# Kernel tuning notes

Measured on AMD Instinct MI355X. Metric: run time of the kernel, lower is better.

The kernel has to match this reference:

```python
import jax, jax.numpy as jnp
from jax import lax
import numpy as np

B, A, T = 128, 32, 32
HID = 64
DEG = 7
MODES = 25
OUT_FRAMES = 12
NHEAD, DHEAD = 16, 64


def legendre_tmat(out_frames, degree):
    # normalized Legendre basis evaluated at t_n, shape [degree+1, len(t_n)]
    t = np.arange(-6, out_frames + 1, dtype=np.float32)
    t = t / t[-1]
    P = [np.ones_like(t), t]
    for n in range(1, degree):
        P.append(((2 * n + 1) * t * P[n] - n * P[n - 1]) / (n + 1))
    P = np.stack(P[: degree + 1], 0)
    norm = np.sqrt((2 * np.arange(degree + 1) + 1) / 2.0).astype(np.float32)
    return (P * norm[:, None]).astype(np.float32)


def _conv(x, w, stride, pad):
    return lax.conv_general_dilated(x, w, (stride, stride), [(pad, pad), (pad, pad)],
                                    dimension_numbers=("NCHW", "OIHW", "NCHW"))


def _bn(x, g, b, eps=1e-5):
    m = jnp.mean(x, axis=(0, 2, 3), keepdims=True)
    v = jnp.var(x, axis=(0, 2, 3), keepdims=True)
    return (x - m) / jnp.sqrt(v + eps) * g[None, :, None, None] + b[None, :, None, None]


def setup_inputs() -> dict:
    key = jax.random.key(0)
    ks = jax.random.split(key, 32)

    def rn(i, shape, scale=0.05):
        return jax.random.normal(ks[i], shape, dtype=jnp.float32) * scale

    inp = {
        "cnn_feat": rn(0, (B, 1024, 14, 14), 1.0),
        "ego_state": rn(1, (B, T, 5), 1.0),
        "agents_state": rn(2, (B, A, T, 5), 1.0),
        "ego_state_len": jax.random.randint(ks[3], (B,), 0, T),
        "agents_state_len": jax.random.randint(ks[4], (B, A), 0, T),
        "agents_grid_pos": jax.random.randint(ks[5], (B, A, 2), 0, 14),
        "state_fc_W": rn(6, (HID, 5)), "state_fc_b": rn(7, (HID,)),
        "lstm_Wih": rn(8, (4 * HID, HID)), "lstm_Whh": rn(9, (4 * HID, HID)),
        "lstm_bih": rn(10, (4 * HID,)), "lstm_bhh": rn(11, (4 * HID,)),
        "enc_fc_W": rn(12, (HID, HID)), "enc_fc_b": rn(13, (HID,)),
        "conv1_W": rn(14, (512, 1024 + HID, 3, 3)),
        "bn1_g": jnp.ones((512,), jnp.float32), "bn1_b": jnp.zeros((512,), jnp.float32),
        "conv2_W": rn(15, (512, 512, 3, 3)),
        "bn2_g": jnp.ones((512,), jnp.float32), "bn2_b": jnp.zeros((512,), jnp.float32),
        "q_W": rn(16, (NHEAD * DHEAD, 512 + HID)),
        "k_W": rn(17, (NHEAD * DHEAD, 512, 1, 1)),
        "v_W": rn(18, (NHEAD * DHEAD, 512, 1, 1)),
        "attn_out_W": rn(19, (512, NHEAD * DHEAD)), "attn_out_b": rn(20, (512,)),
        "cls_W": rn(21, (MODES, 512 + HID + 512)), "cls_b": rn(22, (MODES,)),
        "dec1_W": rn(23, (256, 512 + HID + 512)), "dec1_b": rn(24, (256,)),
        "dec2_W": rn(25, ((DEG + 1) * 2 * MODES, 256)), "dec2_b": rn(26, ((DEG + 1) * 2 * MODES,)),
    }
    return inp


def reference(cnn_feat, ego_state, agents_state, ego_state_len, agents_state_len,
              agents_grid_pos, state_fc_W, state_fc_b, lstm_Wih, lstm_Whh, lstm_bih,
              lstm_bhh, enc_fc_W, enc_fc_b, conv1_W, bn1_g, bn1_b, conv2_W, bn2_g,
              bn2_b, q_W, k_W, v_W, attn_out_W, attn_out_b, cls_W, cls_b, dec1_W,
              dec1_b, dec2_W, dec2_b):
    Bn, _, Hs, Ws = cnn_feat.shape

    def lstm_encode(seq, lens):
        # seq [N,T,5]; packed-sequence semantics with zero init == take h at step len-1
        N, Tn, _ = seq.shape
        h = seq @ state_fc_W.T + state_fc_b  # [N,T,64]

        def step(carry, xt):
            hh, cc = carry
            g = xt @ lstm_Wih.T + hh @ lstm_Whh.T + lstm_bih + lstm_bhh
            i, f_, gg, o = jnp.split(g, 4, axis=-1)
            cc = jax.nn.sigmoid(f_) * cc + jax.nn.sigmoid(i) * jnp.tanh(gg)
            hh = jax.nn.sigmoid(o) * jnp.tanh(cc)
            return (hh, cc), hh

        z = jnp.zeros((N, HID), h.dtype)
        _, hs = lax.scan(step, (z, z), h.transpose(1, 0, 2))  # hs [T,N,64]
        idx = jnp.clip(lens, 1, Tn).astype(jnp.int32) - 1
        last = hs[idx, jnp.arange(N)]
        return last @ enc_fc_W.T + enc_fc_b

    ego = lstm_encode(ego_state, ego_state_len)  # [B,64]
    ag = lstm_encode(agents_state.reshape(Bn * A, T, 5),
                     agents_state_len.reshape(-1)).reshape(Bn, A, HID)

    # scatter-add agent encodings into the spatial grid (overlapping writes accumulate)
    grid = jnp.zeros((Bn, Hs, Ws, HID), cnn_feat.dtype)
    bidx = jnp.broadcast_to(jnp.arange(Bn)[:, None], (Bn, A))
    grid = grid.at[bidx, agents_grid_pos[..., 0], agents_grid_pos[..., 1]].add(ag)

    x = jnp.concatenate([cnn_feat, grid.transpose(0, 3, 1, 2)], axis=1)
    x = jax.nn.relu(_bn(_conv(x, conv1_W, 1, 1), bn1_g, bn1_b))
    x = jax.nn.relu(_bn(_conv(x, conv2_W, 2, 1), bn2_g, bn2_b))  # [B,512,7,7]

    ego_t = jnp.concatenate([x[:, :, 3, 3], ego], axis=1)  # [B,576]
    q = (ego_t @ q_W.T).reshape(Bn, NHEAD, DHEAD)
    k = _conv(x, k_W, 1, 1).reshape(Bn, NHEAD, DHEAD, -1)  # g = 9*9 = 81
    v = _conv(x, v_W, 1, 1).reshape(Bn, NHEAD, DHEAD, -1)
    energy = jnp.einsum("bhf,bhfg->bhg", q, k)
    attn = jax.nn.softmax(energy / (NHEAD * DHEAD) ** 0.5, axis=2)
    o = jnp.einsum("bhg,bhdg->bhd", attn, v).reshape(Bn, -1)
    o = o @ attn_out_W.T + attn_out_b

    feat = jnp.concatenate([o, ego_t], axis=1)  # [B,1088]
    conf = feat @ cls_W.T + cls_b
    d = jax.nn.relu(feat @ dec1_W.T + dec1_b)
    d = (d @ dec2_W.T + dec2_b).reshape(Bn, MODES, -1)

    tmat = jnp.asarray(legendre_tmat(OUT_FRAMES, DEG))  # [DEG+1, 19]
    out_x = d[:, :, : DEG + 1] @ tmat
    out_y = d[:, :, DEG + 1:] @ tmat
    traj = jnp.stack([out_x, out_y], axis=3)  # [B,MODES,19,2]
    return traj, conf
```

## Files before the change

kernel.cpp:

```cpp
#include <hip/hip_runtime.h>
#include <stdint.h>
#include <stddef.h>

#define DEVINL static __device__ __forceinline__

typedef __attribute__((ext_vector_type(8))) short  bfrag;
typedef __attribute__((ext_vector_type(4))) float  facc;

DEVINL uint16_t f2b(float f){
  uint32_t u = __float_as_uint(f);
  return (uint16_t)((u + 0x7fffu + ((u >> 16) & 1u)) >> 16);
}
DEVINL float b2f(uint16_t b){ return __uint_as_float(((uint32_t)b) << 16); }

DEVINL facc MFMA(bfrag a, bfrag b, facc c){
  return __builtin_amdgcn_mfma_f32_16x16x32_bf16(a, b, c, 0, 0, 0);
}

DEVINL void gload16(const void* g, void* l){
  __builtin_amdgcn_global_load_lds(
      (const __attribute__((address_space(1))) uint32_t*)g,
      (__attribute__((address_space(3))) uint32_t*)l, 16, 0, 0);
}

DEVINL float fast_tanh(float x){
  return 2.f/(1.f+__expf(-2.f*x)) - 1.f;
}

struct F2BJobs {
  const float* s[7];
  uint16_t*    d[7];
  int          n[7];
};
__global__ void k_f2b_multi(F2BJobs jobs){
  int j = blockIdx.y;
  const float* s = jobs.s[j];
  uint16_t* d = jobs.d[j];
  int n = jobs.n[j];
  int i = blockIdx.x*256 + threadIdx.x;
  int st = gridDim.x*256;
  for(; i<n; i+=st) d[i] = f2b(s[i]);
}

__global__ void k_zborder(uint16_t* __restrict__ X, uint16_t* __restrict__ Y){
  int b = blockIdx.x & 127, t = threadIdx.x;
  uint16_t* base = (blockIdx.x < 128) ? X : Y;
  int C = (blockIdx.x < 128) ? 1088 : 512;
  for(int p=0;p<60;p++){
    int y, x;
    if(p<16){ y=0; x=p; }
    else if(p<32){ y=15; x=p-16; }
    else { int q=p-32; y=1+(q>>1); x=(q&1)?15:0; }
    uint32_t* dst = (uint32_t*)(base + ((size_t)(b*16+y)*16 + x)*C);
    for(int i=t;i<C/2;i+=256) dst[i] = 0;
  }
}

__global__ void k_lstm_prep(const float* __restrict__ Wih, const float* __restrict__ Whh,
                            const float* __restrict__ bih, const float* __restrict__ bhh,
                            const float* __restrict__ sW, const float* __restrict__ sb,
                            const float* __restrict__ encW,
                            uint16_t* __restrict__ Wc, float* __restrict__ be,
                            uint16_t* __restrict__ encWb, float* __restrict__ tm){
  int n = threadIdx.x;
  if(n < 19){
    float tv = (float)(n - 6) / 12.0f;
    float Pm = 1.0f, Pc = tv;
    tm[0*19+n] = Pm * sqrtf(0.5f);
    tm[1*19+n] = Pc * sqrtf(1.5f);
    for(int q=1; q<7; q++){
      float Pn = ((float)(2*q+1)*tv*Pc - (float)q*Pm) / (float)(q+1);
      Pm = Pc; Pc = Pn;
      tm[(q+1)*19+n] = Pc * sqrtf((float)(2*(q+1)+1) * 0.5f);
    }
  }
  for(int k=0;k<64;k++) Wc[n*96+k] = f2b(Whh[n*64+k]);
  for(int k5=0;k5<5;k5++){
    float s = 0.f;
    for(int j=0;j<64;j++) s += Wih[n*64+j]*sW[j*5+k5];
    Wc[n*96+64+k5] = f2b(s);
  }
  for(int k=69;k<96;k++) Wc[n*96+k] = 0;
  float s = 0.f;
  for(int j=0;j<64;j++) s += Wih[n*64+j]*sb[j];
  be[n] = s + bih[n] + bhh[n];
  if(n < 64){
    for(int k=0;k<64;k++) encWb[n*64+k] = f2b(encW[n*64+k]);
  }
}

__global__ __launch_bounds__(256) void k_lstm(
    const float* __restrict__ ego_seq, const float* __restrict__ ag_seq,
    const int* __restrict__ ego_len, const int* __restrict__ ag_len,
    const int* __restrict__ grid_pos,
    const uint16_t* __restrict__ Wc, const float* __restrict__ be,
    const uint16_t* __restrict__ encWb, const float* __restrict__ encB,
    float* __restrict__ agrid, uint16_t* __restrict__ egoT, uint16_t* __restrict__ feat)
{
  __shared__ __align__(16) uint16_t A[32*96];
  __shared__ float Xf[32*160];
  __shared__ int   idxs[32];

  int t = threadIdx.x, w = t>>6, l = t&63;
  int blk = blockIdx.x;
  bool isEgo = blk < 4;
  int seq0 = isEgo ? blk*32 : (blk-4)*32;
  const float* seqp = (isEgo ? ego_seq : ag_seq) + (size_t)seq0*160;

  for(int i=t;i<32*160;i+=256) Xf[i] = seqp[i];
  if(t < 32){
    int L = isEgo ? ego_len[seq0+t] : ag_len[seq0+t];
    if(L < 1) L = 1;
    idxs[t] = L-1;
  }
  for(int i=t;i<32*96;i+=256) A[i] = 0;

  bfrag bf[4][3];
  float be4[4];
  for(int ct=0;ct<4;ct++){
    int n = (ct*4+w)*16 + (l&15);
    for(int ks=0;ks<3;ks++)
      bf[ct][ks] = *(const bfrag*)(Wc + n*96 + ks*32 + (l>>4)*8);
    be4[ct] = be[n];
  }
  float cst[8], hl[8];
  for(int i=0;i<8;i++){ cst[i]=0.f; hl[i]=0.f; }
  __syncthreads();
  int myidx[8];
  for(int rt=0;rt<2;rt++) for(int r=0;r<4;r++){
    int s = rt*16 + (l>>4)*4 + r;
    myidx[rt*4+r] = idxs[s];
  }

  for(int st=0; st<32; st++){
    if(t < 160){ int s=t/5, kk=t%5; A[s*96+64+kk] = f2b(Xf[s*160 + st*5 + kk]); }
    __syncthreads();
    facc acc[2][4];
    for(int rt=0;rt<2;rt++) for(int ct=0;ct<4;ct++) acc[rt][ct] = facc{0.f,0.f,0.f,0.f};
    #pragma unroll
    for(int ks=0;ks<3;ks++){
      bfrag aA[2];
      #pragma unroll
      for(int rt=0;rt<2;rt++)
        aA[rt] = *(const bfrag*)(A + (rt*16+(l&15))*96 + ks*32 + (l>>4)*8);
      #pragma unroll
      for(int rt=0;rt<2;rt++)
        #pragma unroll
        for(int ct=0;ct<4;ct++)
          acc[rt][ct] = MFMA(aA[rt], bf[ct][ks], acc[rt][ct]);
    }
    __syncthreads();
    #pragma unroll
    for(int rt=0;rt<2;rt++) for(int r=0;r<4;r++){
      int cell = rt*4+r;
      int s = rt*16 + (l>>4)*4 + r;
      float gi = acc[rt][0][r] + be4[0];
      float gf = acc[rt][1][r] + be4[1];
      float gg = acc[rt][2][r] + be4[2];
      float go = acc[rt][3][r] + be4[3];
      float si = 1.f/(1.f+__expf(-gi));
      float sf = 1.f/(1.f+__expf(-gf));
      float so = 1.f/(1.f+__expf(-go));
      float tg = fast_tanh(gg);
      float c2 = sf*cst[cell] + si*tg;
      cst[cell] = c2;
      float hn = so*fast_tanh(c2);
      A[s*96 + w*16 + (l&15)] = f2b(hn);
      if(st == myidx[cell]) hl[cell] = hn;
    }
  }
  __syncthreads();
  for(int rt=0;rt<2;rt++) for(int r=0;r<4;r++){
    int s = rt*16 + (l>>4)*4 + r;
    A[s*96 + w*16 + (l&15)] = f2b(hl[rt*4+r]);
  }
  __syncthreads();
  bfrag eb[2];
  for(int ks=0;ks<2;ks++)
    eb[ks] = *(const bfrag*)(encWb + (w*16+(l&15))*64 + ks*32 + (l>>4)*8);
  facc ea[2]; ea[0] = facc{0.f,0.f,0.f,0.f}; ea[1] = facc{0.f,0.f,0.f,0.f};
  for(int ks=0;ks<2;ks++){
    for(int rt=0;rt<2;rt++){
      bfrag aA = *(const bfrag*)(A + (rt*16+(l&15))*96 + ks*32 + (l>>4)*8);
      ea[rt] = MFMA(aA, eb[ks], ea[rt]);
    }
  }
  int n = w*16 + (l&15);
  float bn_ = encB[n];
  for(int rt=0;rt<2;rt++) for(int r=0;r<4;r++){
    int s = rt*16 + (l>>4)*4 + r;
    float v = ea[rt][r] + bn_;
    int gs = seq0 + s;
    if(isEgo){
      egoT[(size_t)gs*576 + 512 + n] = f2b(v);
      feat[(size_t)gs*1088 + 1024 + n] = f2b(v);
    } else {
      int py = grid_pos[gs*2+0], px = grid_pos[gs*2+1];
      atomicAdd(&agrid[((size_t)(gs>>5)*196 + py*14 + px)*64 + n], v);
    }
  }
}

__global__ void k_packx(const float* __restrict__ cnn, const float* __restrict__ agrid,
                        uint16_t* __restrict__ Xp)
{
  __shared__ float tile[32*200];
  int b = blockIdx.x, ch = blockIdx.y, t = threadIdx.x;
  if(ch < 32){
    int c0 = ch*32;
    for(int i=t;i<32*196;i+=256){
      int ci = i/196, s = i%196;
      tile[ci*200+s] = cnn[((size_t)b*1024 + c0+ci)*196 + s];
    }
    __syncthreads();
    for(int i=t;i<32*196;i+=256){
      int s = i>>5, ci = i&31;
      int y = s/14, x = s%14;
      Xp[(((size_t)b*16 + y+1)*16 + x+1)*1088 + c0 + ci] = f2b(tile[ci*200+s]);
    }
  } else {
    int j0 = (ch-32)*32;
    for(int i=t;i<32*196;i+=256){
      int s = i>>5, ji = i&31;
      int y = s/14, x = s%14;
      Xp[(((size_t)b*16 + y+1)*16 + x+1)*1088 + 1024 + j0 + ji] =
          f2b(agrid[((size_t)b*196 + s)*64 + j0 + ji]);
    }
  }
}

__global__ void k_packw(const float* __restrict__ W, uint16_t* __restrict__ Wp, int O, int C)
{
  int o = blockIdx.x;
  int c = blockIdx.y*64 + threadIdx.x;
  const float* src = W + ((size_t)o*C + c)*9;
  float v[9];
  #pragma unroll
  for(int d=0;d<9;d++) v[d] = src[d];
  #pragma unroll
  for(int d=0;d<9;d++)
    Wp[((size_t)d*O + o)*C + c] = f2b(v[d]);
}

__global__ void k_packw2(const float* __restrict__ W, uint16_t* __restrict__ Wp)
{
  int o = blockIdx.x;
  int c = blockIdx.y*64 + threadIdx.x;
  const float* src = W + ((size_t)o*512 + c)*9;
  float v[9];
  #pragma unroll
  for(int d=0;d<9;d++) v[d] = src[d];
  #pragma unroll
  for(int dy=0;dy<3;dy++)
    #pragma unroll
    for(int dx=0;dx<3;dx++)
      Wp[((size_t)(dy*512 + o))*1536 + dx*512 + c] = f2b(v[dy*3+dx]);
}

__global__ __launch_bounds__(512) void k_conv1_8p(
    const uint16_t* __restrict__ Ain, const uint16_t* __restrict__ Wb,
    uint16_t* __restrict__ Out, float* __restrict__ stats)
{
  constexpr int CB = 1088;
  constexpr int NSTEP = 153;
  __shared__ __align__(16) char LDSb[131072];

  int t = threadIdx.x, w = t>>6, l = t&63;
  int wm = w>>2, wn = w&3;

  int xcd = blockIdx.x & 7, pos = blockIdx.x >> 3;
  int wgid = (xcd < 4 ? xcd*25 : 100 + (xcd-4)*24) + pos;
  int m0 = (wgid % 98) * 256;
  int n0 = (wgid / 98) * 256;

  const uint16_t* aP[2][2];
  const uint16_t* bP[2][2];
  #pragma unroll
  for(int P=0;P<2;P++)
    #pragma unroll
    for(int j=0;j<2;j++){
      int partrow = j*64 + (t>>3);
      int swz = ((t&7) ^ (partrow&7))*8;
      int gr = P*64 + partrow + ((partrow>=64)?64:0);
      int m = m0 + gr; int b = m/196, s = m%196, y = s/14, x = s%14;
      aP[P][j] = Ain + ((b*16+y)*16+x)*CB + swz;
      int nb = n0 + (partrow>>5)*64 + P*32 + (partrow&31);
      bP[P][j] = Wb + (size_t)nb*CB + swz;
    }

  facc acc[8][4];
  #pragma unroll
  for(int i=0;i<8;i++)
    #pragma unroll
    for(int j=0;j<4;j++) acc[i][j] = facc{0.f,0.f,0.f,0.f};

  int dd = 0;

  #define STG(buf, PART) do{                                                   \
    if((PART)==0 || (PART)==3){ const int P_ = ((PART)==3);                    \
      _Pragma("unroll")                                                        \
      for(int j_=0;j_<2;j_++)                                                  \
        gload16(aP[P_][j_], LDSb + (buf)*65536 + P_*16384 + j_*8192 + w*1024); \
    } else { const int P_ = ((PART)==2);                                       \
      _Pragma("unroll")                                                        \
      for(int j_=0;j_<2;j_++)                                                  \
        gload16(bP[P_][j_], LDSb + (buf)*65536 + 32768 + P_*16384 + j_*8192 + w*1024); \
    }                                                                          \
  }while(0)

  #define ADVK() do{                                                          \
    if(dd==8){                                                                \
      _Pragma("unroll")                                                       \
      for(int P_=0;P_<2;P_++) for(int j_=0;j_<2;j_++){                        \
        aP[P_][j_] += 64 - 34*CB; bP[P_][j_] += 64 - 8*512*CB; }              \
      dd = 0;                                                                 \
    } else {                                                                  \
      int sA_ = (dd==2||dd==5) ? 14*CB : CB;                                  \
      _Pragma("unroll")                                                       \
      for(int P_=0;P_<2;P_++) for(int j_=0;j_<2;j_++){                        \
        aP[P_][j_] += sA_; bP[P_][j_] += 512*CB; }                            \
      dd++;                                                                   \
    }                                                                         \
  }while(0)

  #define VM4 asm volatile("s_waitcnt vmcnt(4)" ::: "memory")
  #define VM2 asm volatile("s_waitcnt vmcnt(2)" ::: "memory")
  #define VM0 asm volatile("s_waitcnt vmcnt(0)" ::: "memory")

  #define PHASE(mh, nh, SP, DO_STG, WAIT) do{                                 \
    const uint16_t* Ab_ = (const uint16_t*)(LDSb + p*65536 + (mh)*16384);     \
    const uint16_t* Bb_ = (const uint16_t*)(LDSb + p*65536 + 32768 + (nh)*16384); \
    bfrag a_[4][2], b_[2][2];                                                 \
    _Pragma("unroll")                                                         \
    for(int i_=0;i_<4;i_++)                                                   \
      _Pragma("unroll")                                                       \
      for(int ks_=0;ks_<2;ks_++)                                              \
        a_[i_][ks_] = *(const bfrag*)(Ab_ + (wm*64 + i_*16 + (l&15))*64       \
                        + ((ks_*32 + (l>>4)*8) ^ ((l&7)<<3)));                \
    _Pragma("unroll")                                                         \
    for(int j_=0;j_<2;j_++)                                                   \
      _Pragma("unroll")                                                       \
      for(int ks_=0;ks_<2;ks_++)                                              \
        b_[j_][ks_] = *(const bfrag*)(Bb_ + (wn*32 + j_*16 + (l&15))*64       \
                        + ((ks_*32 + (l>>4)*8) ^ ((l&7)<<3)));                \
    if(DO_STG) STG(p^1, SP);                                                  \
    __builtin_amdgcn_sched_barrier(0);                                        \
    __builtin_amdgcn_s_barrier();                                             \
    __builtin_amdgcn_s_setprio(1);                                            \
    _Pragma("unroll")                                                         \
    for(int ks_=0;ks_<2;ks_++)                                                \
      _Pragma("unroll")                                                       \
      for(int i_=0;i_<4;i_++)                                                 \
        _Pragma("unroll")                                                     \
        for(int j_=0;j_<2;j_++)                                               \
          acc[(mh)*4+i_][(nh)*2+j_] =                                         \
            MFMA(a_[i_][ks_], b_[j_][ks_], acc[(mh)*4+i_][(nh)*2+j_]);        \
    __builtin_amdgcn_s_setprio(0);                                            \
    WAIT;                                                                     \
    __builtin_amdgcn_s_barrier();                                             \
  }while(0)

  STG(0,0); STG(0,1); STG(0,2); STG(0,3);
  ADVK();
  VM4;
  __builtin_amdgcn_s_barrier();

  for(int kt=0; kt<NSTEP-1; kt++){
    int p = kt&1;
    PHASE(0,0, 0, 1, VM4);
    PHASE(0,1, 1, 1, VM4);
    PHASE(1,0, 2, 1, (void)0);
    PHASE(1,1, 3, 1, VM4);
    if(kt < NSTEP-2) ADVK();
  }
  {
    int p = 0;
    PHASE(0,0, 0, 0, VM2);
    PHASE(0,1, 1, 0, VM0);
    PHASE(1,0, 2, 0, (void)0);
    PHASE(1,1, 3, 0, (void)0);
  }

  #undef PHASE
  #undef STG
  #undef ADVK

  __syncthreads();
  int* oo = (int*)LDSb;
  if(t < 256){
    int m = m0 + t; int b = m/196, s = m%196, y = s/14, x = s%14;
    oo[t] = ((b*16 + y+1)*16 + (x+1))*512;
  }
  __syncthreads();
  #pragma unroll
  for(int i=0;i<8;i++)
    #pragma unroll
    for(int j=0;j<4;j++){
      int n = n0 + wn*64 + j*16 + (l&15);
      #pragma unroll
      for(int r=0;r<4;r++){
        int mr = wm*128 + i*16 + (l>>4)*4 + r;
        Out[(size_t)oo[mr] + n] = f2b(acc[i][j][r]);
      }
    }
  __syncthreads();
  float* sred = (float*)LDSb;
  int rg = wm*4 + (l>>4);
  #pragma unroll
  for(int j=0;j<4;j++){
    float s=0.f, q=0.f;
    #pragma unroll
    for(int i=0;i<8;i++)
      #pragma unroll
      for(int r=0;r<4;r++){ float v = acc[i][j][r]; s += v; q += v*v; }
    int nl = wn*64 + j*16 + (l&15);
    sred[(nl*8 + rg)*2+0] = s;
    sred[(nl*8 + rg)*2+1] = q;
  }
  __syncthreads();
  if(t < 256){
    float s=0.f, q=0.f;
    #pragma unroll
    for(int rgi=0;rgi<8;rgi++){ s += sred[(t*8+rgi)*2]; q += sred[(t*8+rgi)*2+1]; }
    atomicAdd(&stats[n0+t], s);
    atomicAdd(&stats[512+n0+t], q);
  }
}

__global__ __launch_bounds__(256) void k_conv2dy(
    const uint16_t* __restrict__ Ain, const uint16_t* __restrict__ Wb,
    float* __restrict__ PS)
{
  __shared__ __align__(16) uint16_t As[128*64];
  __shared__ __align__(16) uint16_t Bs[128*64];

  int t = threadIdx.x, w = t>>6, l = t&63;
  int dy = blockIdx.y;

  int xcd = blockIdx.x & 7, pos = blockIdx.x >> 3;
  int wgid = (xcd < 4 ? xcd*25 : 100 + (xcd-4)*24) + pos;
  int n0 = (wgid / 49) * 128;
  int m0 = (wgid % 49) * 128;

  const uint16_t* aP[4];
  const uint16_t* bP[4];
  #pragma unroll
  for(int p=0;p<4;p++){
    int r = w*32 + p*8 + (l>>3);
    int m = m0 + r;
    int b = m/49, s = m%49, y = s/7, x = s%7;
    aP[p] = Ain + ((b*16 + 2*y + dy)*16 + 2*x)*512 + (l&7)*8;
    bP[p] = Wb + ((size_t)(dy*512 + n0 + r))*1536 + (l&7)*8;
  }

  facc acc[4][4];
  #pragma unroll
  for(int i=0;i<4;i++)
    #pragma unroll
    for(int j=0;j<4;j++) acc[i][j] = facc{0.f,0.f,0.f,0.f};
  int wm = w>>1, wn = w&1;
  char* asDst = (char*)As + w*4096;
  char* bsDst = (char*)Bs + w*4096;

  for(int stp=0; stp<24; stp++){
    #pragma unroll
    for(int p=0;p<4;p++){ gload16(aP[p], asDst + p*1024); aP[p] += 64; }
    #pragma unroll
    for(int p=0;p<4;p++){ gload16(bP[p], bsDst + p*1024); bP[p] += 64; }
    __syncthreads();
    #pragma unroll
    for(int ks=0;ks<2;ks++){
      bfrag a[4], b[4];
      #pragma unroll
      for(int i=0;i<4;i++)
        a[i] = *(const bfrag*)(As + (wm*64 + i*16 + (l&15))*64 + ks*32 + (l>>4)*8);
      #pragma unroll
      for(int j=0;j<4;j++)
        b[j] = *(const bfrag*)(Bs + (wn*64 + j*16 + (l&15))*64 + ks*32 + (l>>4)*8);
      #pragma unroll
      for(int i=0;i<4;i++)
        #pragma unroll
        for(int j=0;j<4;j++)
          acc[i][j] = MFMA(a[i], b[j], acc[i][j]);
    }
    __syncthreads();
  }

  float* out = PS + (size_t)dy*3211264;
  #pragma unroll
  for(int i=0;i<4;i++)
    #pragma unroll
    for(int j=0;j<4;j++){
      int n = n0 + wn*64 + j*16 + (l&15);
      #pragma unroll
      for(int r=0;r<4;r++){
        int mr = m0 + wm*64 + i*16 + (l>>4)*4 + r;
        out[(size_t)mr*512 + n] = acc[i][j][r];
      }
    }
}

__global__ void k_bn2sum(const float* __restrict__ PS, uint16_t* __restrict__ Y2,
                         float* __restrict__ stats)
{
  int t = threadIdx.x;
  int m0 = blockIdx.x*128;
  float s0=0,s1=0,q0=0,q1=0;
  for(int i=0;i<128;i++){
    size_t off = (size_t)(m0+i)*512 + 2*t;
    float2 p0 = *(const float2*)(PS + off);
    float2 p1 = *(const float2*)(PS + 3211264 + off);
    float2 p2 = *(const float2*)(PS + 6422528 + off);
    float a = p0.x+p1.x+p2.x, c = p0.y+p1.y+p2.y;
    s0+=a; q0+=a*a; s1+=c; q1+=c*c;
    *(uint32_t*)(Y2 + off) = (uint32_t)f2b(a) | ((uint32_t)f2b(c)<<16);
  }
  atomicAdd(&stats[2*t],   s0);
  atomicAdd(&stats[2*t+1], s1);
  atomicAdd(&stats[512+2*t],   q0);
  atomicAdd(&stats[512+2*t+1], q1);
}

__global__ __launch_bounds__(256) void k_convkv(
    const uint16_t* __restrict__ Ain, const uint16_t* __restrict__ Wb,
    uint16_t* __restrict__ Out)
{
  constexpr int CB = 512;
  constexpr int NB = 2048;
  constexpr int NWG = 49*16;
  constexpr int Q8 = NWG/8;

  __shared__ __align__(16) uint16_t As[128*64];
  __shared__ __align__(16) uint16_t Bs[128*64];

  int t = threadIdx.x, w = t>>6, l = t&63;

  int xcd = blockIdx.x & 7, pos = blockIdx.x >> 3;
  int wgid = xcd*Q8 + pos;
  int n0 = (wgid / 49) * 128;
  int m0 = (wgid % 49) * 128;

  const uint16_t* aP[4];
  const uint16_t* bP[4];
  #pragma unroll
  for(int p=0;p<4;p++){
    int r = w*32 + p*8 + (l>>3);
    aP[p] = Ain + (size_t)(m0 + r)*512 + (l&7)*8;
    bP[p] = Wb + (size_t)(n0 + r)*CB + (l&7)*8;
  }

  facc acc[4][4];
  #pragma unroll
  for(int i=0;i<4;i++)
    #pragma unroll
    for(int j=0;j<4;j++) acc[i][j] = facc{0.f,0.f,0.f,0.f};
  int wm = w>>1, wn = w&1;
  char* asDst = (char*)As + w*4096;
  char* bsDst = (char*)Bs + w*4096;

  for(int cc=0; cc<8; cc++){
    #pragma unroll
    for(int p=0;p<4;p++){ gload16(aP[p], asDst + p*1024); aP[p] += 64; }
    #pragma unroll
    for(int p=0;p<4;p++){ gload16(bP[p], bsDst + p*1024); bP[p] += 64; }
    __syncthreads();
    #pragma unroll
    for(int ks=0;ks<2;ks++){
      bfrag a[4], b[4];
      #pragma unroll
      for(int i=0;i<4;i++)
        a[i] = *(const bfrag*)(As + (wm*64 + i*16 + (l&15))*64 + ks*32 + (l>>4)*8);
      #pragma unroll
      for(int j=0;j<4;j++)
        b[j] = *(const bfrag*)(Bs + (wn*64 + j*16 + (l&15))*64 + ks*32 + (l>>4)*8);
      #pragma unroll
      for(int i=0;i<4;i++)
        #pragma unroll
        for(int j=0;j<4;j++)
          acc[i][j] = MFMA(a[i], b[j], acc[i][j]);
    }
    __syncthreads();
  }

  #pragma unroll
  for(int i=0;i<4;i++)
    #pragma unroll
    for(int j=0;j<4;j++){
      int n = n0 + wn*64 + j*16 + (l&15);
      #pragma unroll
      for(int r=0;r<4;r++){
        int mr = m0 + wm*64 + i*16 + (l>>4)*4 + r;
        Out[(size_t)mr*2048 + n] = f2b(acc[i][j][r]);
      }
    }
}

template<int PAD>
__global__ void k_bnapply(uint16_t* __restrict__ Y, const float* __restrict__ stats,
                          const float* __restrict__ gg, const float* __restrict__ bb,
                          int M, float invM,
                          uint16_t* __restrict__ egoT, uint16_t* __restrict__ feat)
{
  int t = threadIdx.x;
  int m0 = blockIdx.x*8;
  float mu0 = stats[2*t]*invM,       mu1 = stats[2*t+1]*invM;
  float v0 = stats[512+2*t]*invM - mu0*mu0, v1 = stats[512+2*t+1]*invM - mu1*mu1;
  float sc0 = gg[2*t]  *rsqrtf(v0+1e-5f), sc1 = gg[2*t+1]*rsqrtf(v1+1e-5f);
  float sh0 = bb[2*t]   - mu0*sc0,        sh1 = bb[2*t+1] - mu1*sc1;
  for(int i=0;i<8;i++){
    int m = m0+i; if(m>=M) break;
    size_t off;
    if(PAD){ int b=m/196, s=m%196, y=s/14, x=s%14; off = (((size_t)b*16+y+1)*16 + x+1)*512; }
    else off = (size_t)m*512;
    uint32_t u = *(const uint32_t*)(Y + off + 2*t);
    float a = fmaxf(b2f((uint16_t)u)*sc0 + sh0, 0.f);
    float c = fmaxf(b2f((uint16_t)(u>>16))*sc1 + sh1, 0.f);
    uint32_t pu = (uint32_t)f2b(a) | ((uint32_t)f2b(c)<<16);
    *(uint32_t*)(Y + off + 2*t) = pu;
    if(!PAD && (m%49)==24){
      int b = m/49;
      *(uint32_t*)(egoT + (size_t)b*576 + 2*t) = pu;
      *(uint32_t*)(feat + (size_t)b*1088 + 512 + 2*t) = pu;
    }
  }
}

__global__ __launch_bounds__(256) void k_sgemm(
    const uint16_t* __restrict__ A, int lda,
    const uint16_t* __restrict__ B, int ldb,
    const float* __restrict__ bias,
    void* __restrict__ C, int ldc,
    int N, int K, int flags)
{
  int t = threadIdx.x, w = t>>6, l = t&63;
  int nt = blockIdx.x*4 + w;
  int n  = nt*16 + (l&15);
  int m0 = blockIdx.y*16;
  bool nv = n < N;
  facc acc = facc{0.f,0.f,0.f,0.f};
  for(int k=0;k<K;k+=32){
    bfrag af = *(const bfrag*)(A + (size_t)(m0+(l&15))*lda + k + (l>>4)*8);
    bfrag bf_ = {0,0,0,0,0,0,0,0};
    if(nv) bf_ = *(const bfrag*)(B + (size_t)n*ldb + k + (l>>4)*8);
    acc = MFMA(af, bf_, acc);
  }
  if(nv){
    float bv = bias ? bias[n] : 0.f;
    #pragma unroll
    for(int r=0;r<4;r++){
      int m = m0 + (l>>4)*4 + r;
      float v = acc[r] + bv;
      if(flags & 1) v = fmaxf(v, 0.f);
      if(flags & 2) ((float*)C)[(size_t)m*ldc + n] = v;
      else ((uint16_t*)C)[(size_t)m*ldc + n] = f2b(v);
    }
  }
}

__global__ __launch_bounds__(256) void k_attn(
    const float* __restrict__ q, const uint16_t* __restrict__ kv,
    uint16_t* __restrict__ o)
{
  int t = threadIdx.x, w = t>>6, l = t&63;
  int idx = blockIdx.x*4 + w;
  int b = idx>>4, h = idx&15;
  float qf = q[(size_t)b*1024 + h*64 + l];
  const uint16_t* kp = kv + (size_t)b*49*2048 + h*64 + l;
  float eo = 0.f;
  for(int g=0; g<49; g++){
    float p = qf * b2f(kp[(size_t)g*2048]);
    for(int s=32;s>0;s>>=1) p += __shfl_xor(p, s);
    if(l == g) eo = p;
  }
  float e = (l<49) ? eo*(1.f/32.f) : -1e30f;
  float mx = e;
  for(int s=32;s>0;s>>=1) mx = fmaxf(mx, __shfl_xor(mx, s));
  mx = fmaxf(mx, 0.f);
  float p = (l<49) ? __expf(e-mx) : 0.f;
  float den = p;
  for(int s=32;s>0;s>>=1) den += __shfl_xor(den, s);
  den += 32.f*__expf(-mx);
  const uint16_t* vp = kv + (size_t)b*49*2048 + 1024 + h*64 + l;
  float accv = 0.f;
  for(int g=0; g<49; g++){
    float pg = __shfl(p, g);
    accv += pg * b2f(vp[(size_t)g*2048]);
  }
  o[(size_t)b*1024 + h*64 + l] = f2b(accv/den);
}

__global__ void k_traj(const float* __restrict__ d2, const float* __restrict__ tm,
                       float* __restrict__ out)
{
  int i = blockIdx.x*256 + threadIdx.x;
  if(i >= 3200) return;
  const float* dp = d2 + (size_t)i*16;
  float cx[8], cy[8];
  #pragma unroll
  for(int j=0;j<8;j++){ cx[j]=dp[j]; cy[j]=dp[8+j]; }
  float* op = out + (size_t)i*38;
  for(int tt=0;tt<19;tt++){
    float x=0.f, y=0.f;
    #pragma unroll
    for(int j=0;j<8;j++){ float tv = tm[j*19+tt]; x += cx[j]*tv; y += cy[j]*tv; }
    op[tt*2+0]=x; op[tt*2+1]=y;
  }
}

extern "C" void kernel_launch(void* const* d_in, const int* in_sizes, int n_in,
                              void* d_out, int out_size, void* d_ws, size_t ws_size,
                              hipStream_t stream)
{
  const float* cnn      = (const float*)d_in[0];
  const float* ego_seq  = (const float*)d_in[1];
  const float* ag_seq   = (const float*)d_in[2];
  const int*   ego_len  = (const int*)d_in[3];
  const int*   ag_len   = (const int*)d_in[4];
  const int*   grid_pos = (const int*)d_in[5];
  const float* sW  = (const float*)d_in[6];
  const float* sb  = (const float*)d_in[7];
  const float* Wih = (const float*)d_in[8];
  const float* Whh = (const float*)d_in[9];
  const float* bih = (const float*)d_in[10];
  const float* bhh = (const float*)d_in[11];
  const float* encW = (const float*)d_in[12];
  const float* encB = (const float*)d_in[13];
  const float* conv1W = (const float*)d_in[14];
  const float* bn1g = (const float*)d_in[15];
  const float* bn1b = (const float*)d_in[16];
  const float* conv2W = (const float*)d_in[17];
  const float* bn2g = (const float*)d_in[18];
  const float* bn2b = (const float*)d_in[19];
  const float* qWf  = (const float*)d_in[20];
  const float* kWf  = (const float*)d_in[21];
  const float* vWf  = (const float*)d_in[22];
  const float* aoW  = (const float*)d_in[23];
  const float* aoB  = (const float*)d_in[24];
  const float* clsWf = (const float*)d_in[25];
  const float* clsB  = (const float*)d_in[26];
  const float* d1Wf  = (const float*)d_in[27];
  const float* d1B   = (const float*)d_in[28];
  const float* d2Wf  = (const float*)d_in[29];
  const float* d2B   = (const float*)d_in[30];

  char* ws = (char*)d_ws;
  const size_t XP_OFF   = 0;
  const size_t PS_OFF   = 0;
  const size_t KV_OFF   = 0;
  const size_t Y2_OFF   = 41943040;
  const size_t Y1P_OFF  = 71303168;
  const size_t WP1_OFF  = 104857600;
  const size_t WP2_OFF  = 114884608;
  const size_t WKV_OFF  = 119603200;
  const size_t QW_OFF   = 121700352;
  const size_t AOW_OFF  = 122880000;
  const size_t CLSW_OFF = 123928576;
  const size_t D1W_OFF  = 123982976;
  const size_t D2W_OFF  = 124540032;
  const size_t GRID_OFF = 124744832;
  const size_t EGOT_OFF = 131167360;
  const size_t FEAT_OFF = 131314816;
  const size_t QBUF_OFF = 131593344;
  const size_t OBUF_OFF = 132117632;
  const size_t D1_OFF   = 132379776;
  const size_t D2_OFF   = 132445312;
  const size_t WC_OFF   = 132650112;
  const size_t BE_OFF   = 132699264;
  const size_t ENCW_OFF = 132700288;
  const size_t TMAT_OFF = 132708480;
  const size_t ST1_OFF  = 132709120;
  const size_t ST2_OFF  = 132713216;

  uint16_t* XP   = (uint16_t*)(ws + XP_OFF);
  float*    PS   = (float*)(ws + PS_OFF);
  uint16_t* KV   = (uint16_t*)(ws + KV_OFF);
  uint16_t* Y2   = (uint16_t*)(ws + Y2_OFF);
  uint16_t* Y1P  = (uint16_t*)(ws + Y1P_OFF);
  uint16_t* WP1  = (uint16_t*)(ws + WP1_OFF);
  uint16_t* WP2  = (uint16_t*)(ws + WP2_OFF);
  uint16_t* WKV  = (uint16_t*)(ws + WKV_OFF);
  uint16_t* QW   = (uint16_t*)(ws + QW_OFF);
  uint16_t* AOW  = (uint16_t*)(ws + AOW_OFF);
  uint16_t* CLSW = (uint16_t*)(ws + CLSW_OFF);
  uint16_t* D1W  = (uint16_t*)(ws + D1W_OFF);
  uint16_t* D2W  = (uint16_t*)(ws + D2W_OFF);
  float*    GRIDB= (float*)(ws + GRID_OFF);
  uint16_t* EGOT = (uint16_t*)(ws + EGOT_OFF);
  uint16_t* FEAT = (uint16_t*)(ws + FEAT_OFF);
  float*    QBUF = (float*)(ws + QBUF_OFF);
  uint16_t* OBUF = (uint16_t*)(ws + OBUF_OFF);
  uint16_t* D1B  = (uint16_t*)(ws + D1_OFF);
  float*    D2B  = (float*)(ws + D2_OFF);
  uint16_t* WC   = (uint16_t*)(ws + WC_OFF);
  float*    BE   = (float*)(ws + BE_OFF);
  uint16_t* ENCWB= (uint16_t*)(ws + ENCW_OFF);
  float*    TMAT = (float*)(ws + TMAT_OFF);
  float*    ST1  = (float*)(ws + ST1_OFF);
  float*    ST2  = (float*)(ws + ST2_OFF);
  float*    outF = (float*)d_out;

  (void)hipMemsetAsync(ws + GRID_OFF, 0, 6422528, stream);
  (void)hipMemsetAsync(ws + ST1_OFF,  0, 8192, stream);

  k_zborder<<<256,256,0,stream>>>(XP, Y1P);

  k_lstm_prep<<<1,256,0,stream>>>(Wih,Whh,bih,bhh,sW,sb,encW, WC,BE,ENCWB, TMAT);
  k_packw<<<dim3(512,17),64,0,stream>>>(conv1W, WP1, 512, 1088);
  k_packw2<<<dim3(512,8),64,0,stream>>>(conv2W, WP2);
  {
    F2BJobs jb;
    jb.s[0]=kWf;  jb.d[0]=WKV;              jb.n[0]=1024*512;
    jb.s[1]=vWf;  jb.d[1]=WKV + 1024*512;   jb.n[1]=1024*512;
    jb.s[2]=qWf;  jb.d[2]=QW;               jb.n[2]=1024*576;
    jb.s[3]=aoW;  jb.d[3]=AOW;              jb.n[3]=512*1024;
    jb.s[4]=clsWf;jb.d[4]=CLSW;             jb.n[4]=25*1088;
    jb.s[5]=d1Wf; jb.d[5]=D1W;              jb.n[5]=256*1088;
    jb.s[6]=d2Wf; jb.d[6]=D2W;              jb.n[6]=400*256;
    k_f2b_multi<<<dim3(48,7),256,0,stream>>>(jb);
  }

  k_lstm<<<132,256,0,stream>>>(ego_seq, ag_seq, ego_len, ag_len, grid_pos,
                               WC, BE, ENCWB, encB, GRIDB, EGOT, FEAT);
  k_packx<<<dim3(128,34),256,0,stream>>>(cnn, GRIDB, XP);
  k_conv1_8p<<<196,512,0,stream>>>(XP, WP1, Y1P, ST1);
  k_bnapply<1><<<3136,256,0,stream>>>(Y1P, ST1, bn1g, bn1b, 25088, 1.f/25088.f, nullptr, nullptr);
  k_conv2dy<<<dim3(196,3),256,0,stream>>>(Y1P, WP2, PS);
  k_bn2sum<<<49,256,0,stream>>>(PS, Y2, ST2);
  k_bnapply<0><<<784,256,0,stream>>>(Y2, ST2, bn2g, bn2b, 6272, 1.f/6272.f, EGOT, FEAT);
  k_convkv<<<784,256,0,stream>>>(Y2, WKV, KV);
  k_sgemm<<<dim3(16,8),256,0,stream>>>(EGOT, 576, QW, 576, nullptr, QBUF, 1024, 1024, 576, 2);
  k_attn<<<512,256,0,stream>>>(QBUF, KV, OBUF);
  k_sgemm<<<dim3(8,8),256,0,stream>>>(OBUF, 1024, AOW, 1024, aoB, FEAT, 1088, 512, 1024, 0);
  k_sgemm<<<dim3(1,8),256,0,stream>>>(FEAT, 1088, CLSW, 1088, clsB, outF + 121600, 25, 25, 1088, 2);
  k_sgemm<<<dim3(4,8),256,0,stream>>>(FEAT, 1088, D1W, 1088, d1B, D1B, 256, 256, 1088, 1);
  k_sgemm<<<dim3(7,8),256,0,stream>>>(D1B, 256, D2W, 256, d2B, D2B, 400, 400, 256, 2);
  k_traj<<<13,256,0,stream>>>(D2B, TMAT, outF);

  (void)in_sizes; (void)n_in; (void)out_size; (void)ws_size;
}
```

Baseline: 664.3 us.

## Reuse LDS fragments across conv1 phases and spread bn2 reduction over more blocks

The conv1 GEMM main loop is split into separate A/B fragment loads and MFMA steps. Phases now run in a snake order (00, 01, 11, 10), so each phase reloads only one of the A or B fragments from LDS instead of both, which cuts LDS read traffic. Separately, the bn2 partial-sum kernel now handles 16 rows per block across 392 blocks instead of 128 rows across 49 blocks, raising parallelism at the cost of more atomics on the stats buffer. An unused constant is also removed.

```diff
diff --git a/kernel.cpp b/kernel.cpp
--- a/kernel.cpp
+++ b/kernel.cpp
@@ -294,6 +294,7 @@
     #pragma unroll
     for(int j=0;j<4;j++) acc[i][j] = facc{0.f,0.f,0.f,0.f};
 
+  bfrag aF[4][2], bF[2][2];
   int dd = 0;
 
   #define STG(buf, PART) do{                                                   \
@@ -327,25 +328,27 @@
   #define VM2 asm volatile("s_waitcnt vmcnt(2)" ::: "memory")
   #define VM0 asm volatile("s_waitcnt vmcnt(0)" ::: "memory")
 
-  #define PHASE(mh, nh, SP, DO_STG, WAIT) do{                                 \
+  #define LDA(mh) do{                                                         \
     const uint16_t* Ab_ = (const uint16_t*)(LDSb + p*65536 + (mh)*16384);     \
-    const uint16_t* Bb_ = (const uint16_t*)(LDSb + p*65536 + 32768 + (nh)*16384); \
-    bfrag a_[4][2], b_[2][2];                                                 \
     _Pragma("unroll")                                                         \
     for(int i_=0;i_<4;i_++)                                                   \
       _Pragma("unroll")                                                       \
       for(int ks_=0;ks_<2;ks_++)                                              \
-        a_[i_][ks_] = *(const bfrag*)(Ab_ + (wm*64 + i_*16 + (l&15))*64       \
+        aF[i_][ks_] = *(const bfrag*)(Ab_ + (wm*64 + i_*16 + (l&15))*64       \
                         + ((ks_*32 + (l>>4)*8) ^ ((l&7)<<3)));                \
+  }while(0)
+
+  #define LDB(nh) do{                                                         \
+    const uint16_t* Bb_ = (const uint16_t*)(LDSb + p*65536 + 32768 + (nh)*16384); \
     _Pragma("unroll")                                                         \
     for(int j_=0;j_<2;j_++)                                                   \
       _Pragma("unroll")                                                       \
       for(int ks_=0;ks_<2;ks_++)                                              \
-        b_[j_][ks_] = *(const bfrag*)(Bb_ + (wn*32 + j_*16 + (l&15))*64       \
+        bF[j_][ks_] = *(const bfrag*)(Bb_ + (wn*32 + j_*16 + (l&15))*64       \
                         + ((ks_*32 + (l>>4)*8) ^ ((l&7)<<3)));                \
-    if(DO_STG) STG(p^1, SP);                                                  \
-    __builtin_amdgcn_sched_barrier(0);                                        \
-    __builtin_amdgcn_s_barrier();                                             \
+  }while(0)
+
+  #define MM(mh, nh) do{                                                      \
     __builtin_amdgcn_s_setprio(1);                                            \
     _Pragma("unroll")                                                         \
     for(int ks_=0;ks_<2;ks_++)                                                \
@@ -354,34 +357,39 @@
         _Pragma("unroll")                                                     \
         for(int j_=0;j_<2;j_++)                                               \
           acc[(mh)*4+i_][(nh)*2+j_] =                                         \
-            MFMA(a_[i_][ks_], b_[j_][ks_], acc[(mh)*4+i_][(nh)*2+j_]);        \
+            MFMA(aF[i_][ks_], bF[j_][ks_], acc[(mh)*4+i_][(nh)*2+j_]);        \
     __builtin_amdgcn_s_setprio(0);                                            \
-    WAIT;                                                                     \
-    __builtin_amdgcn_s_barrier();                                             \
   }while(0)
+
+  #define BARS do{ __builtin_amdgcn_sched_barrier(0); __builtin_amdgcn_s_barrier(); }while(0)
+  #define EBAR __builtin_amdgcn_s_barrier()
 
   STG(0,0); STG(0,1); STG(0,2); STG(0,3);
   ADVK();
   VM4;
-  __builtin_amdgcn_s_barrier();
+  EBAR;
 
   for(int kt=0; kt<NSTEP-1; kt++){
     int p = kt&1;
-    PHASE(0,0, 0, 1, VM4);
-    PHASE(0,1, 1, 1, VM4);
-    PHASE(1,0, 2, 1, (void)0);
-    PHASE(1,1, 3, 1, VM4);
+    LDA(0); LDB(0); STG(p^1,0); BARS; MM(0,0); VM4; EBAR;
+    LDB(1);         STG(p^1,1); BARS; MM(0,1); VM4; EBAR;
+    LDA(1);         STG(p^1,2); BARS; MM(1,1);      EBAR;
+    LDB(0);         STG(p^1,3); BARS; MM(1,0); VM4; EBAR;
     if(kt < NSTEP-2) ADVK();
   }
   {
     int p = 0;
-    PHASE(0,0, 0, 0, VM2);
-    PHASE(0,1, 1, 0, VM0);
-    PHASE(1,0, 2, 0, (void)0);
-    PHASE(1,1, 3, 0, (void)0);
-  }
-
-  #undef PHASE
+    LDA(0); LDB(0); BARS; MM(0,0); VM2; EBAR;
+    LDB(1);         BARS; MM(0,1); VM0; EBAR;
+    LDA(1);         BARS; MM(1,1);      EBAR;
+    LDB(0);         BARS; MM(1,0);      EBAR;
+  }
+
+  #undef LDA
+  #undef LDB
+  #undef MM
+  #undef BARS
+  #undef EBAR
   #undef STG
   #undef ADVK
 
@@ -504,9 +512,9 @@
                          float* __restrict__ stats)
 {
   int t = threadIdx.x;
-  int m0 = blockIdx.x*128;
+  int m0 = blockIdx.x*16;
   float s0=0,s1=0,q0=0,q1=0;
-  for(int i=0;i<128;i++){
+  for(int i=0;i<16;i++){
     size_t off = (size_t)(m0+i)*512 + 2*t;
     float2 p0 = *(const float2*)(PS + off);
     float2 p1 = *(const float2*)(PS + 3211264 + off);
@@ -526,7 +534,6 @@
     uint16_t* __restrict__ Out)
 {
   constexpr int CB = 512;
-  constexpr int NB = 2048;
   constexpr int NWG = 49*16;
   constexpr int Q8 = NWG/8;
 
@@ -825,7 +832,7 @@
   k_conv1_8p<<<196,512,0,stream>>>(XP, WP1, Y1P, ST1);
   k_bnapply<1><<<3136,256,0,stream>>>(Y1P, ST1, bn1g, bn1b, 25088, 1.f/25088.f, nullptr, nullptr);
   k_conv2dy<<<dim3(196,3),256,0,stream>>>(Y1P, WP2, PS);
-  k_bn2sum<<<49,256,0,stream>>>(PS, Y2, ST2);
+  k_bn2sum<<<392,256,0,stream>>>(PS, Y2, ST2);
   k_bnapply<0><<<784,256,0,stream>>>(Y2, ST2, bn2g, bn2b, 6272, 1.f/6272.f, EGOT, FEAT);
   k_convkv<<<784,256,0,stream>>>(Y2, WKV, KV);
   k_sgemm<<<dim3(16,8),256,0,stream>>>(EGOT, 576, QW, 576, nullptr, QBUF, 1024, 1024, 576, 2);
```

After: 629.6 us. 1.06x faster.
